# Kernel optimization log

Hardware: AMD Instinct MI355X
Metric: run time of the kernel (lower is better)

The kernel has to match this reference:

```python
import jax, jax.numpy as jnp
import numpy as np


def _sobel(img):
    # replicate-pad then Sobel cross-correlation (matches torch conv2d with wx, wy)
    p = jnp.pad(img, ((0, 0), (0, 0), (1, 1), (1, 1)), mode='edge')
    dx = ((p[:, :, 0:-2, 2:] - p[:, :, 0:-2, 0:-2])
          + 2.0 * (p[:, :, 1:-1, 2:] - p[:, :, 1:-1, 0:-2])
          + (p[:, :, 2:, 2:] - p[:, :, 2:, 0:-2]))
    dy = ((p[:, :, 2:, 0:-2] - p[:, :, 0:-2, 0:-2])
          + 2.0 * (p[:, :, 2:, 1:-1] - p[:, :, 0:-2, 1:-1])
          + (p[:, :, 2:, 2:] - p[:, :, 0:-2, 2:]))
    return dx, dy


def _compute_normal(vertex):
    # normal = normalize(dV/dx x dV/dy); zero out pixels at global min/max depth
    dx, dy = _sobel(vertex)
    n = jnp.cross(dx, dy, axis=1)                      # [B,3,H,W]
    mag = jnp.sqrt(jnp.sum(n * n, axis=1, keepdims=True) + 1e-16)
    n = n / (mag + 1e-8)
    depth = vertex[:, 2:3]
    invalid = (depth == depth.min()) | (depth == depth.max())
    return jnp.where(invalid, 0.0, n)


def _warp(feat, u, v):
    # bilinear sampling of feat [B,C,H,W] at (u,v) [B,N] -> [B,C,N]
    B, C, H, W = feat.shape
    u = jnp.clip(u, 0.0, W - 1.0)
    v = jnp.clip(v, 0.0, H - 1.0)
    u0 = jnp.floor(u); v0 = jnp.floor(v)
    wu = u - u0; wv = v - v0
    u0i = u0.astype(jnp.int32); v0i = v0.astype(jnp.int32)
    u1i = jnp.minimum(u0i + 1, W - 1); v1i = jnp.minimum(v0i + 1, H - 1)
    flat = feat.reshape(B, C, H * W)
    N = u.shape[-1]
    def g(ui, vi):
        idx = (vi * W + ui)[:, None, :]
        return jnp.take_along_axis(flat, jnp.broadcast_to(idx, (B, C, N)), axis=2)
    return (g(u0i, v0i) * ((1 - wu) * (1 - wv))[:, None]
            + g(u1i, v0i) * (wu * (1 - wv))[:, None]
            + g(u0i, v1i) * ((1 - wu) * wv)[:, None]
            + g(u1i, v1i) * (wu * wv)[:, None])


def _skew(v):  # [B,3] -> [B,3,3]
    x, y, z = v[..., 0], v[..., 1], v[..., 2]
    O = jnp.zeros_like(x)
    return jnp.stack([jnp.stack([O, -z, y], -1),
                      jnp.stack([z, O, -x], -1),
                      jnp.stack([-y, x, O], -1)], -2)


def _twist2mat(w):  # Rodrigues: so(3) [B,3] -> SO(3) [B,3,3]
    th = jnp.sqrt(jnp.sum(w * w, -1, keepdims=True) + 1e-24)
    Kv = _skew(w / th)
    th = th[..., None]
    I = jnp.eye(3, dtype=w.dtype)
    return I + jnp.sin(th) * Kv + (1.0 - jnp.cos(th)) * (Kv @ Kv)


def _icp_forward(depth0, depth1, K, R, t, max_iter=3):
    B, _, H, W = depth0.shape
    fx, fy, cx, cy = [K[:, i:i + 1] for i in range(4)]  # each [B,1]
    uu = jnp.arange(W, dtype=depth0.dtype)
    vv = jnp.arange(H, dtype=depth0.dtype)
    px = (uu[None, None, None, :] - cx[:, :, None, None]) / fx[:, :, None, None]
    py = (vv[None, None, :, None] - cy[:, :, None, None]) / fy[:, :, None, None]
    px = jnp.broadcast_to(px, (B, 1, H, W))
    py = jnp.broadcast_to(py, (B, 1, H, W))
    vertex0 = jnp.concatenate([px * depth0, py * depth0, depth0], 1)  # [B,3,H,W]
    vertex1 = jnp.concatenate([px * depth1, py * depth1, depth1], 1)
    normal0 = _compute_normal(vertex0)
    normal1 = _compute_normal(vertex1)
    N = H * W
    V0 = vertex0.reshape(B, 3, N)
    N0 = normal0.reshape(B, 3, N)
    P0 = V0.transpose(0, 2, 1)                          # [B,N,3]
    dpt0 = vertex0[:, 2].reshape(B, N)
    sigma_z = 0.0012 + 0.0019 * (dpt0 - 0.4) ** 2       # depth noise model
    eye6 = jnp.eye(6, dtype=depth0.dtype)
    for _ in range(max_iter):
        v0to1 = R @ V0 + t                               # [B,3,N]
        x_, y_, s_ = v0to1[:, 0], v0to1[:, 1], v0to1[:, 2]
        u_ = x_ / s_ * fx + cx
        v_ = y_ / s_ * fy + cy
        inviews = (u_ > 0) & (u_ < W - 1) & (v_ > 0) & (v_ < H - 1)
        rV1 = _warp(vertex1, u_, v_)                     # [B,3,N]
        rN1 = _warp(normal1, u_, v_)
        diff = v0to1 - rV1
        dnorm = jnp.sqrt(jnp.sum(diff * diff, axis=1) + 1e-16)
        occ = (~inviews) | (dnorm > 0.1)                 # [B,N]
        res = jnp.sum(rN1 * diff, axis=1)                # point-to-plane residual [B,N]
        NtC = jnp.einsum('bcn,bck->bnk', rN1, R)         # n_r^T R, [B,N,3]
        # n^T [p]_x == cross(n^T R, p)
        J = jnp.concatenate([jnp.cross(NtC, P0), -NtC], -1)  # [B,N,6]
        # sigma ~ |n_r . (R e_z)| * sigma_z (depth noise projected on normal)
        ndot = jnp.abs(jnp.sum(rN1 * R[:, :, 2][:, :, None], axis=1))
        sigma = ndot * sigma_z + 1e-3
        w_res = res / (sigma + 1e-8)
        J = -J / (sigma + 1e-8)[..., None]
        w_res = jnp.where(occ, 0.0, w_res)
        J = jnp.where(occ[..., None], 0.0, J)
        JtWJ = jnp.einsum('bnk,bnl->bkl', J, J)          # [B,6,6]
        JtR = jnp.einsum('bnk,bn->bk', J, w_res)[..., None]  # [B,6,1]
        tr = jnp.trace(JtWJ, axis1=1, axis2=2)
        Hlm = JtWJ + (tr * 1e-6)[:, None, None] * eye6   # LM damping
        xi = jnp.linalg.inv(Hlm) @ JtR                   # [B,6,1]
        dR = _twist2mat(-xi[:, :3, 0])
        dt = -(dR @ xi[:, 3:])
        R, t = R @ dR, R @ dt + t                        # inverse-compositional update
    weights = jnp.ones((B, 1, H, W), dtype=depth0.dtype)
    return R, t, weights


def setup_inputs() -> dict:
    key = jax.random.key(0)
    B, H, W = 16, 480, 640
    k1, k2, k3, k4 = jax.random.split(key, 4)
    TWO_PI = 6.2831853
    xs = jnp.linspace(0.0, 1.0, W, dtype=jnp.float32)
    ys = jnp.linspace(0.0, 1.0, H, dtype=jnp.float32)
    phase = jax.random.uniform(k1, (B, 1, 1, 1), minval=0.0, maxval=TWO_PI)
    # smooth positive depth surface so ICP inlier test keeps valid pixels
    depth0 = (2.0 + 0.5 * jnp.sin(TWO_PI * 3.0 * xs[None, None, None, :] + phase)
              * jnp.cos(TWO_PI * 2.0 * ys[None, None, :, None])).astype(jnp.float32)
    depth1 = depth0 + 0.01 * jax.random.normal(k2, (B, 1, H, W), dtype=jnp.float32)
    K = jnp.tile(jnp.array([[525.0, 525.0, 319.5, 239.5]], dtype=jnp.float32), (B, 1))
    w = 0.005 * jax.random.normal(k3, (B, 3), dtype=jnp.float32)
    R = _twist2mat(w)                                    # near-identity initial rotation
    t = 0.005 * jax.random.normal(k4, (B, 3, 1), dtype=jnp.float32)
    return {"depth0": depth0, "depth1": depth1, "K": K, "R": R, "t": t}


def reference(depth0, depth1, K, R, t):
    return _icp_forward(depth0, depth1, K, R, t, max_iter=3)
```

## Files before the change

### kernel.cpp

```cpp
#include <hip/hip_runtime.h>
#include <hip/hip_fp16.h>

#define IMH 480
#define IMW 640
#define HW (IMH*IMW)
#define NB 16

#define BPB 100
#define TPX 4
#define GROUPS 3
#define THREADS_PB (BPB*256)
#define GSTRIDE (THREADS_PB*TPX)
#define GROWS (GSTRIDE/IMW)

__device__ inline unsigned fenc(float x){
    unsigned u = __float_as_uint(x);
    return (u & 0x80000000u) ? ~u : (u | 0x80000000u);
}
__device__ inline float fdec(unsigned e){
    unsigned u = (e & 0x80000000u) ? (e & 0x7FFFFFFFu) : ~e;
    return __uint_as_float(u);
}

__global__ void init_kernel(const float* __restrict__ Rin, const float* __restrict__ tin,
                            float* __restrict__ stateR, float* __restrict__ statet,
                            unsigned* __restrict__ mm, float* __restrict__ acc){
    int i = threadIdx.x;
    if (i < NB*9) stateR[i] = Rin[i];
    if (i < NB*3) statet[i] = tin[i];
    if (i == 0){ mm[0] = 0xFFFFFFFFu; mm[1] = 0u; }
    for (int k = i; k < NB*27; k += 256) acc[k] = 0.f;
}

__global__ __launch_bounds__(256) void minmax_kernel(const float4* __restrict__ d, unsigned* __restrict__ mm){
    unsigned lmin = 0xFFFFFFFFu, lmax = 0u;
    const int total4 = NB*HW/4;
    for (int i = blockIdx.x*256 + threadIdx.x; i < total4; i += gridDim.x*256){
        float4 v = d[i];
        unsigned e0 = fenc(v.x), e1 = fenc(v.y), e2 = fenc(v.z), e3 = fenc(v.w);
        lmin = min(lmin, min(min(e0,e1), min(e2,e3)));
        lmax = max(lmax, max(max(e0,e1), max(e2,e3)));
    }
    #pragma unroll
    for (int off = 32; off; off >>= 1){
        lmin = min(lmin, (unsigned)__shfl_down((int)lmin, off));
        lmax = max(lmax, (unsigned)__shfl_down((int)lmax, off));
    }
    __shared__ unsigned smin[4], smax[4];
    int wave = threadIdx.x >> 6, lane = threadIdx.x & 63;
    if (lane == 0){ smin[wave] = lmin; smax[wave] = lmax; }
    __syncthreads();
    if (threadIdx.x == 0){
        unsigned bmin = min(min(smin[0],smin[1]), min(smin[2],smin[3]));
        unsigned bmax = max(max(smax[0],smax[1]), max(smax[2],smax[3]));
        atomicMin(&mm[0], bmin);
        atomicMax(&mm[1], bmax);
    }
}

__global__ __launch_bounds__(256) void normal_kernel(const float* __restrict__ depth1,
                                                     const float* __restrict__ Kp,
                                                     const unsigned* __restrict__ mm,
                                                     uint2* __restrict__ nrm,
                                                     float* __restrict__ weights){
    int b = blockIdx.y;
    int pix = blockIdx.x*256 + threadIdx.x;
    int r = pix / IMW, c = pix % IMW;
    const float fx = Kp[b*4+0], fy = Kp[b*4+1], cx = Kp[b*4+2], cy = Kp[b*4+3];
    const float inv_fx = 1.f/fx, inv_fy = 1.f/fy;
    const float* __restrict__ d = depth1 + (size_t)b*HW;
    int rm = max(r-1,0), rp = min(r+1,IMH-1), cm = max(c-1,0), cp = min(c+1,IMW-1);

    auto vert = [&](int rr, int cc, float v[3]){
        float dd = d[rr*IMW+cc];
        v[0] = ((float)cc - cx)*inv_fx*dd;
        v[1] = ((float)rr - cy)*inv_fy*dd;
        v[2] = dd;
    };
    float va[3],vb[3],vc2[3],vd[3],ve[3],vf[3],vg[3],vh[3];
    vert(rm,cm,va); vert(rm,c,vb);  vert(rm,cp,vc2);
    vert(r ,cm,vd);                 vert(r ,cp,ve);
    vert(rp,cm,vf); vert(rp,c,vg);  vert(rp,cp,vh);

    float dx[3], dy[3];
    #pragma unroll
    for (int k=0;k<3;k++){
        dx[k] = (vc2[k]-va[k]) + 2.f*(ve[k]-vd[k]) + (vh[k]-vf[k]);
        dy[k] = (vf[k]-va[k]) + 2.f*(vg[k]-vb[k]) + (vh[k]-vc2[k]);
    }
    float nx = dx[1]*dy[2] - dx[2]*dy[1];
    float ny = dx[2]*dy[0] - dx[0]*dy[2];
    float nz = dx[0]*dy[1] - dx[1]*dy[0];
    float mag = sqrtf(nx*nx + ny*ny + nz*nz + 1e-16f);
    float inv = __builtin_amdgcn_rcpf(mag + 1e-8f);
    nx *= inv; ny *= inv; nz *= inv;

    float dc = d[r*IMW+c];
    float dmin = fdec(mm[0]), dmax = fdec(mm[1]);
    if (dc == dmin || dc == dmax){ nx = 0.f; ny = 0.f; nz = 0.f; }

    __half2 hxy = __floats2half2_rn(nx, ny);
    __half2 hz0 = __floats2half2_rn(nz, 0.f);
    uint2 p;
    p.x = *reinterpret_cast<unsigned*>(&hxy);
    p.y = *reinterpret_cast<unsigned*>(&hz0);
    nrm[(size_t)b*HW + pix] = p;
    weights[(size_t)b*HW + pix] = 1.f;
}

__global__ __launch_bounds__(256) void iter_kernel(const float4* __restrict__ depth0_v4,
                                                   const float* __restrict__ depth1,
                                                   const uint2* __restrict__ nrm,
                                                   const float* __restrict__ Kp,
                                                   const float* __restrict__ stateR,
                                                   const float* __restrict__ statet,
                                                   float* __restrict__ acc){
    const int b = blockIdx.y;
    const float fx = Kp[b*4+0], fy = Kp[b*4+1], cx = Kp[b*4+2], cy = Kp[b*4+3];
    const float inv_fx = 1.f/fx, inv_fy = 1.f/fy;
    float Rm[9];
    #pragma unroll
    for (int i=0;i<9;i++) Rm[i] = stateR[b*9+i];
    float tv[3];
    #pragma unroll
    for (int i=0;i<3;i++) tv[i] = statet[b*3+i];

    const float4* __restrict__ d0v = depth0_v4 + (size_t)b*(HW/4);
    const float* __restrict__ d1   = depth1 + (size_t)b*HW;
    const uint2* __restrict__ nb_  = nrm + (size_t)b*HW;

    float accv[27];
    #pragma unroll
    for (int i=0;i<27;i++) accv[i] = 0.f;

    const int tid = blockIdx.x*256 + threadIdx.x;
    const int base0 = tid*TPX;
    const int c0 = base0 % IMW;
    const int r0 = base0 / IMW;
    const float px_base = ((float)c0 - cx)*inv_fx;
    float pyv = ((float)r0 - cy)*inv_fy;
    const float py_step = (float)GROWS*inv_fy;

    #pragma unroll 1
    for (int g = 0; g < GROUPS; g++){
        float4 d4 = d0v[tid + g*THREADS_PB];
        float dd[4] = {d4.x, d4.y, d4.z, d4.w};

        #pragma unroll
        for (int j = 0; j < TPX; j++){
            float d0 = dd[j];
            float V0x = (px_base + (float)j*inv_fx)*d0;
            float V0y = pyv*d0;
            float V0z = d0;

            float X = Rm[0]*V0x + Rm[1]*V0y + Rm[2]*V0z + tv[0];
            float Y = Rm[3]*V0x + Rm[4]*V0y + Rm[5]*V0z + tv[1];
            float Z = Rm[6]*V0x + Rm[7]*V0y + Rm[8]*V0z + tv[2];
            float invZ = __builtin_amdgcn_rcpf(Z);
            float uu = X*invZ*fx + cx;
            float vv = Y*invZ*fy + cy;

            bool inview = (uu > 0.f) && (uu < (float)(IMW-1)) && (vv > 0.f) && (vv < (float)(IMH-1));

            float J0=0.f,J1=0.f,J2=0.f,J3=0.f,J4=0.f,J5=0.f,wres=0.f;
            if (inview){
                float u0f = floorf(uu), v0f = floorf(vv);
                int u0 = (int)u0f, v0 = (int)v0f;
                float wu = uu - u0f, wv = vv - v0f;
                float w00 = (1.f-wu)*(1.f-wv), w10 = wu*(1.f-wv), w01 = (1.f-wu)*wv, w11 = wu*wv;
                int i00 = v0*IMW + u0;

                float d00 = d1[i00], d10 = d1[i00+1], d01 = d1[i00+IMW], d11 = d1[i00+IMW+1];
                uint2 h00 = nb_[i00], h10 = nb_[i00+1], h01 = nb_[i00+IMW], h11 = nb_[i00+IMW+1];

                float pxa = (u0f - cx)*inv_fx, pxb = pxa + inv_fx;
                float pya = (v0f - cy)*inv_fy, pyb = pya + inv_fy;
                float a = w00*d00, bb = w10*d10, cc = w01*d01, ee = w11*d11;
                float rVz = (a + bb) + (cc + ee);
                float rVx = (a + cc)*pxa + (bb + ee)*pxb;
                float rVy = (a + bb)*pya + (cc + ee)*pyb;

                float2 n00xy = __half22float2(*reinterpret_cast<__half2*>(&h00.x));
                float2 n00z_ = __half22float2(*reinterpret_cast<__half2*>(&h00.y));
                float2 n10xy = __half22float2(*reinterpret_cast<__half2*>(&h10.x));
                float2 n10z_ = __half22float2(*reinterpret_cast<__half2*>(&h10.y));
                float2 n01xy = __half22float2(*reinterpret_cast<__half2*>(&h01.x));
                float2 n01z_ = __half22float2(*reinterpret_cast<__half2*>(&h01.y));
                float2 n11xy = __half22float2(*reinterpret_cast<__half2*>(&h11.x));
                float2 n11z_ = __half22float2(*reinterpret_cast<__half2*>(&h11.y));

                float n0x = w00*n00xy.x + w10*n10xy.x + w01*n01xy.x + w11*n11xy.x;
                float n0y = w00*n00xy.y + w10*n10xy.y + w01*n01xy.y + w11*n11xy.y;
                float n0z = w00*n00z_.x + w10*n10z_.x + w01*n01z_.x + w11*n11z_.x;

                float dfx = X - rVx, dfy = Y - rVy, dfz = Z - rVz;
                float d2 = dfx*dfx + dfy*dfy + dfz*dfz + 1e-16f;
                if (d2 <= 0.01f){
                    float res = n0x*dfx + n0y*dfy + n0z*dfz;
                    float N0 = n0x*Rm[0] + n0y*Rm[3] + n0z*Rm[6];
                    float N1 = n0x*Rm[1] + n0y*Rm[4] + n0z*Rm[7];
                    float N2 = n0x*Rm[2] + n0y*Rm[5] + n0z*Rm[8];
                    float cr0 = N1*V0z - N2*V0y;
                    float cr1 = N2*V0x - N0*V0z;
                    float cr2 = N0*V0y - N1*V0x;
                    float ndot = fabsf(N2);
                    float dsh = d0 - 0.4f;
                    float sigz = 0.0012f + 0.0019f*dsh*dsh;
                    float sigma = ndot*sigz + 0.001f;
                    float invs = __builtin_amdgcn_rcpf(sigma + 1e-8f);
                    wres = res*invs;
                    J0 = -cr0*invs; J1 = -cr1*invs; J2 = -cr2*invs;
                    J3 =  N0*invs;  J4 =  N1*invs;  J5 =  N2*invs;
                }
            }

            float Jv[6] = {J0,J1,J2,J3,J4,J5};
            int idx = 0;
            #pragma unroll
            for (int k=0;k<6;k++)
                #pragma unroll
                for (int l=k;l<6;l++){ accv[idx] += Jv[k]*Jv[l]; idx++; }
            #pragma unroll
            for (int k=0;k<6;k++){ accv[idx] += Jv[k]*wres; idx++; }
        }

        pyv += py_step;
    }

    #pragma unroll
    for (int i=0;i<27;i++){
        float v = accv[i];
        #pragma unroll
        for (int off=32; off; off >>= 1) v += __shfl_down(v, off);
        accv[i] = v;
    }

    __shared__ float sacc[4][27];
    int wave = threadIdx.x >> 6, lane = threadIdx.x & 63;
    if (lane == 0){
        #pragma unroll
        for (int i=0;i<27;i++) sacc[wave][i] = accv[i];
    }
    __syncthreads();
    if (threadIdx.x < 27){
        float s = sacc[0][threadIdx.x] + sacc[1][threadIdx.x]
                + sacc[2][threadIdx.x] + sacc[3][threadIdx.x];
        atomicAdd(&acc[b*27 + threadIdx.x], s);
    }
}

__global__ void solve_kernel(float* __restrict__ acc,
                             float* __restrict__ stateR, float* __restrict__ statet,
                             float* __restrict__ outR, float* __restrict__ outt){
    int b = threadIdx.x;
    if (b >= NB) return;

    float a27[27];
    for (int i=0;i<27;i++) a27[i] = acc[b*27+i];
    for (int i=0;i<27;i++) acc[b*27+i] = 0.f;

    double A[6][6], rhs[6];
    int idx = 0;
    for (int k=0;k<6;k++)
        for (int l=k;l<6;l++){ A[k][l] = a27[idx]; A[l][k] = a27[idx]; idx++; }
    for (int k=0;k<6;k++) rhs[k] = a27[21+k];

    double tr = 0.0;
    for (int k=0;k<6;k++) tr += A[k][k];
    double lm = tr*1e-6;
    for (int k=0;k<6;k++) A[k][k] += lm;

    double M[6][7];
    for (int i=0;i<6;i++){ for (int j=0;j<6;j++) M[i][j]=A[i][j]; M[i][6]=rhs[i]; }
    for (int col=0; col<6; col++){
        int piv = col; double best = fabs(M[col][col]);
        for (int r2=col+1; r2<6; r2++){
            double v = fabs(M[r2][col]);
            if (v > best){ best = v; piv = r2; }
        }
        if (piv != col)
            for (int j=0;j<7;j++){ double tmp = M[col][j]; M[col][j] = M[piv][j]; M[piv][j] = tmp; }
        double p = M[col][col];
        for (int j=col;j<7;j++) M[col][j] /= p;
        for (int r2=0;r2<6;r2++){
            if (r2 == col) continue;
            double f = M[r2][col];
            for (int j=col;j<7;j++) M[r2][j] -= f*M[col][j];
        }
    }
    double xi[6];
    for (int k=0;k<6;k++) xi[k] = M[k][6];

    double w0 = -xi[0], w1 = -xi[1], w2 = -xi[2];
    double th = sqrt(w0*w0 + w1*w1 + w2*w2 + 1e-24);
    double kx = w0/th, ky = w1/th, kz = w2/th;
    double s = sin(th), cm1 = 1.0 - cos(th);
    double Kv[3][3] = {{0,-kz,ky},{kz,0,-kx},{-ky,kx,0}};
    double K2[3][3];
    for (int i=0;i<3;i++)
        for (int j=0;j<3;j++){
            double acc2 = 0.0;
            for (int k=0;k<3;k++) acc2 += Kv[i][k]*Kv[k][j];
            K2[i][j] = acc2;
        }
    double dR[3][3];
    for (int i=0;i<3;i++)
        for (int j=0;j<3;j++)
            dR[i][j] = (i==j ? 1.0 : 0.0) + s*Kv[i][j] + cm1*K2[i][j];
    double dt[3];
    for (int i=0;i<3;i++)
        dt[i] = -(dR[i][0]*xi[3] + dR[i][1]*xi[4] + dR[i][2]*xi[5]);

    double Ro[3][3];
    for (int i=0;i<3;i++) for (int j=0;j<3;j++) Ro[i][j] = (double)stateR[b*9 + i*3 + j];
    double to[3];
    for (int i=0;i<3;i++) to[i] = (double)statet[b*3+i];

    double Rn[3][3], tn[3];
    for (int i=0;i<3;i++)
        for (int j=0;j<3;j++){
            double acc2 = 0.0;
            for (int k=0;k<3;k++) acc2 += Ro[i][k]*dR[k][j];
            Rn[i][j] = acc2;
        }
    for (int i=0;i<3;i++)
        tn[i] = Ro[i][0]*dt[0] + Ro[i][1]*dt[1] + Ro[i][2]*dt[2] + to[i];

    for (int i=0;i<3;i++)
        for (int j=0;j<3;j++){
            float v = (float)Rn[i][j];
            stateR[b*9 + i*3 + j] = v;
            outR[b*9 + i*3 + j] = v;
        }
    for (int i=0;i<3;i++){
        float v = (float)tn[i];
        statet[b*3+i] = v;
        outt[b*3+i] = v;
    }
}

extern "C" void kernel_launch(void* const* d_in, const int* in_sizes, int n_in,
                              void* d_out, int out_size, void* d_ws, size_t ws_size,
                              hipStream_t stream){
    const float* depth0 = (const float*)d_in[0];
    const float* depth1 = (const float*)d_in[1];
    const float* Kp     = (const float*)d_in[2];
    const float* Rin    = (const float*)d_in[3];
    const float* tin    = (const float*)d_in[4];

    float* out     = (float*)d_out;
    float* outR    = out;
    float* outt    = out + NB*9;
    float* weights = out + NB*12;

    uint2* nrm     = (uint2*)d_ws;
    float* stateR  = (float*)(nrm + (size_t)NB*HW);
    float* statet  = stateR + NB*9;
    unsigned* mm   = (unsigned*)(statet + NB*3);
    float* acc     = (float*)(mm + 2);

    init_kernel<<<1, 256, 0, stream>>>(Rin, tin, stateR, statet, mm, acc);
    minmax_kernel<<<dim3(256), 256, 0, stream>>>((const float4*)depth1, mm);
    normal_kernel<<<dim3(HW/256, NB), 256, 0, stream>>>(depth1, Kp, mm, nrm, weights);
    for (int it = 0; it < 3; it++){
        iter_kernel<<<dim3(BPB, NB), 256, 0, stream>>>((const float4*)depth0, depth1, nrm, Kp, stateR, statet, acc);
        solve_kernel<<<1, 64, 0, stream>>>(acc, stateR, statet, outR, outt);
    }
}
```

Baseline: 251.9 us.

## Fuse 6x6 solve into iter kernel via last-block-done counter

```diff
diff --git a/kernel.cpp b/kernel.cpp
--- a/kernel.cpp
+++ b/kernel.cpp
@@ -24,11 +24,13 @@
 
 __global__ void init_kernel(const float* __restrict__ Rin, const float* __restrict__ tin,
                             float* __restrict__ stateR, float* __restrict__ statet,
-                            unsigned* __restrict__ mm, float* __restrict__ acc){
+                            unsigned* __restrict__ mm, float* __restrict__ acc,
+                            unsigned* __restrict__ cnt){
     int i = threadIdx.x;
     if (i < NB*9) stateR[i] = Rin[i];
     if (i < NB*3) statet[i] = tin[i];
     if (i == 0){ mm[0] = 0xFFFFFFFFu; mm[1] = 0u; }
+    if (i < NB) cnt[i] = 0u;
     for (int k = i; k < NB*27; k += 256) acc[k] = 0.f;
 }
 
@@ -112,9 +114,12 @@
                                                    const float* __restrict__ depth1,
                                                    const uint2* __restrict__ nrm,
                                                    const float* __restrict__ Kp,
-                                                   const float* __restrict__ stateR,
-                                                   const float* __restrict__ statet,
-                                                   float* __restrict__ acc){
+                                                   float* __restrict__ stateR,
+                                                   float* __restrict__ statet,
+                                                   float* __restrict__ acc,
+                                                   unsigned* __restrict__ cnt,
+                                                   float* __restrict__ outR,
+                                                   float* __restrict__ outt){
     const int b = blockIdx.y;
     const float fx = Kp[b*4+0], fy = Kp[b*4+1], cx = Kp[b*4+2], cy = Kp[b*4+3];
     const float inv_fx = 1.f/fx, inv_fy = 1.f/fy;
@@ -242,100 +247,86 @@
         for (int i=0;i<27;i++) sacc[wave][i] = accv[i];
     }
     __syncthreads();
+    float* __restrict__ accp = acc + b*27;
     if (threadIdx.x < 27){
         float s = sacc[0][threadIdx.x] + sacc[1][threadIdx.x]
                 + sacc[2][threadIdx.x] + sacc[3][threadIdx.x];
-        atomicAdd(&acc[b*27 + threadIdx.x], s);
-    }
-}
-
-__global__ void solve_kernel(float* __restrict__ acc,
-                             float* __restrict__ stateR, float* __restrict__ statet,
-                             float* __restrict__ outR, float* __restrict__ outt){
-    int b = threadIdx.x;
-    if (b >= NB) return;
-
-    float a27[27];
-    for (int i=0;i<27;i++) a27[i] = acc[b*27+i];
-    for (int i=0;i<27;i++) acc[b*27+i] = 0.f;
-
-    double A[6][6], rhs[6];
-    int idx = 0;
-    for (int k=0;k<6;k++)
-        for (int l=k;l<6;l++){ A[k][l] = a27[idx]; A[l][k] = a27[idx]; idx++; }
-    for (int k=0;k<6;k++) rhs[k] = a27[21+k];
-
-    double tr = 0.0;
-    for (int k=0;k<6;k++) tr += A[k][k];
-    double lm = tr*1e-6;
-    for (int k=0;k<6;k++) A[k][k] += lm;
-
-    double M[6][7];
-    for (int i=0;i<6;i++){ for (int j=0;j<6;j++) M[i][j]=A[i][j]; M[i][6]=rhs[i]; }
-    for (int col=0; col<6; col++){
-        int piv = col; double best = fabs(M[col][col]);
-        for (int r2=col+1; r2<6; r2++){
-            double v = fabs(M[r2][col]);
-            if (v > best){ best = v; piv = r2; }
+        atomicAdd(&accp[threadIdx.x], s);
+    }
+    __syncthreads();
+
+    __shared__ float Ms[6][7];
+    if (threadIdx.x == 0){
+        __threadfence();
+        unsigned old = atomicAdd(&cnt[b], 1u);
+        if (old == BPB - 1u){
+            float a27[27];
+            #pragma unroll
+            for (int i=0;i<27;i++) a27[i] = atomicAdd(&accp[i], 0.f);
+            #pragma unroll
+            for (int i=0;i<27;i++) accp[i] = 0.f;
+            cnt[b] = 0u;
+
+            int idx = 0;
+            for (int k=0;k<6;k++)
+                for (int l=k;l<6;l++){ Ms[k][l] = a27[idx]; Ms[l][k] = a27[idx]; idx++; }
+            float tr = 0.f;
+            for (int k=0;k<6;k++) tr += Ms[k][k];
+            float lm = tr*1e-6f;
+            for (int k=0;k<6;k++){ Ms[k][k] += lm; Ms[k][6] = a27[21+k]; }
+
+            for (int col=0; col<6; col++){
+                int piv = col; float best = fabsf(Ms[col][col]);
+                for (int r2=col+1; r2<6; r2++){
+                    float v = fabsf(Ms[r2][col]);
+                    if (v > best){ best = v; piv = r2; }
+                }
+                if (piv != col)
+                    for (int j=0;j<7;j++){ float tmp = Ms[col][j]; Ms[col][j] = Ms[piv][j]; Ms[piv][j] = tmp; }
+                float p = 1.f/Ms[col][col];
+                for (int j=col;j<7;j++) Ms[col][j] *= p;
+                for (int r2=0;r2<6;r2++){
+                    if (r2 == col) continue;
+                    float f = Ms[r2][col];
+                    for (int j=col;j<7;j++) Ms[r2][j] -= f*Ms[col][j];
+                }
+            }
+            float xi[6];
+            for (int k=0;k<6;k++) xi[k] = Ms[k][6];
+
+            float w0 = -xi[0], w1 = -xi[1], w2 = -xi[2];
+            float th = sqrtf(w0*w0 + w1*w1 + w2*w2 + 1e-24f);
+            float ith = 1.f/th;
+            float kx = w0*ith, ky = w1*ith, kz = w2*ith;
+            float s = sinf(th), cm1 = 1.f - cosf(th);
+            float dRm[9];
+            dRm[0] = 1.f + cm1*(-ky*ky - kz*kz);
+            dRm[1] = -s*kz + cm1*(kx*ky);
+            dRm[2] =  s*ky + cm1*(kx*kz);
+            dRm[3] =  s*kz + cm1*(kx*ky);
+            dRm[4] = 1.f + cm1*(-kx*kx - kz*kz);
+            dRm[5] = -s*kx + cm1*(ky*kz);
+            dRm[6] = -s*ky + cm1*(kx*kz);
+            dRm[7] =  s*kx + cm1*(ky*kz);
+            dRm[8] = 1.f + cm1*(-kx*kx - ky*ky);
+
+            float dt0 = -(dRm[0]*xi[3] + dRm[1]*xi[4] + dRm[2]*xi[5]);
+            float dt1 = -(dRm[3]*xi[3] + dRm[4]*xi[4] + dRm[5]*xi[5]);
+            float dt2 = -(dRm[6]*xi[3] + dRm[7]*xi[4] + dRm[8]*xi[5]);
+
+            float Rn[9];
+            for (int i=0;i<3;i++)
+                for (int j=0;j<3;j++)
+                    Rn[i*3+j] = Rm[i*3+0]*dRm[0*3+j] + Rm[i*3+1]*dRm[1*3+j] + Rm[i*3+2]*dRm[2*3+j];
+            float tn0 = Rm[0]*dt0 + Rm[1]*dt1 + Rm[2]*dt2 + tv[0];
+            float tn1 = Rm[3]*dt0 + Rm[4]*dt1 + Rm[5]*dt2 + tv[1];
+            float tn2 = Rm[6]*dt0 + Rm[7]*dt1 + Rm[8]*dt2 + tv[2];
+
+            for (int i=0;i<9;i++){ stateR[b*9+i] = Rn[i]; outR[b*9+i] = Rn[i]; }
+            statet[b*3+0] = tn0; outt[b*3+0] = tn0;
+            statet[b*3+1] = tn1; outt[b*3+1] = tn1;
+            statet[b*3+2] = tn2; outt[b*3+2] = tn2;
         }
-        if (piv != col)
-            for (int j=0;j<7;j++){ double tmp = M[col][j]; M[col][j] = M[piv][j]; M[piv][j] = tmp; }
-        double p = M[col][col];
-        for (int j=col;j<7;j++) M[col][j] /= p;
-        for (int r2=0;r2<6;r2++){
-            if (r2 == col) continue;
-            double f = M[r2][col];
-            for (int j=col;j<7;j++) M[r2][j] -= f*M[col][j];
-        }
-    }
-    double xi[6];
-    for (int k=0;k<6;k++) xi[k] = M[k][6];
-
-    double w0 = -xi[0], w1 = -xi[1], w2 = -xi[2];
-    double th = sqrt(w0*w0 + w1*w1 + w2*w2 + 1e-24);
-    double kx = w0/th, ky = w1/th, kz = w2/th;
-    double s = sin(th), cm1 = 1.0 - cos(th);
-    double Kv[3][3] = {{0,-kz,ky},{kz,0,-kx},{-ky,kx,0}};
-    double K2[3][3];
-    for (int i=0;i<3;i++)
-        for (int j=0;j<3;j++){
-            double acc2 = 0.0;
-            for (int k=0;k<3;k++) acc2 += Kv[i][k]*Kv[k][j];
-            K2[i][j] = acc2;
-        }
-    double dR[3][3];
-    for (int i=0;i<3;i++)
-        for (int j=0;j<3;j++)
-            dR[i][j] = (i==j ? 1.0 : 0.0) + s*Kv[i][j] + cm1*K2[i][j];
-    double dt[3];
-    for (int i=0;i<3;i++)
-        dt[i] = -(dR[i][0]*xi[3] + dR[i][1]*xi[4] + dR[i][2]*xi[5]);
-
-    double Ro[3][3];
-    for (int i=0;i<3;i++) for (int j=0;j<3;j++) Ro[i][j] = (double)stateR[b*9 + i*3 + j];
-    double to[3];
-    for (int i=0;i<3;i++) to[i] = (double)statet[b*3+i];
-
-    double Rn[3][3], tn[3];
-    for (int i=0;i<3;i++)
-        for (int j=0;j<3;j++){
-            double acc2 = 0.0;
-            for (int k=0;k<3;k++) acc2 += Ro[i][k]*dR[k][j];
-            Rn[i][j] = acc2;
-        }
-    for (int i=0;i<3;i++)
-        tn[i] = Ro[i][0]*dt[0] + Ro[i][1]*dt[1] + Ro[i][2]*dt[2] + to[i];
-
-    for (int i=0;i<3;i++)
-        for (int j=0;j<3;j++){
-            float v = (float)Rn[i][j];
-            stateR[b*9 + i*3 + j] = v;
-            outR[b*9 + i*3 + j] = v;
-        }
-    for (int i=0;i<3;i++){
-        float v = (float)tn[i];
-        statet[b*3+i] = v;
-        outt[b*3+i] = v;
     }
 }
 
@@ -358,12 +349,13 @@
     float* statet  = stateR + NB*9;
     unsigned* mm   = (unsigned*)(statet + NB*3);
     float* acc     = (float*)(mm + 2);
-
-    init_kernel<<<1, 256, 0, stream>>>(Rin, tin, stateR, statet, mm, acc);
-    minmax_kernel<<<dim3(256), 256, 0, stream>>>((const float4*)depth1, mm);
+    unsigned* cnt  = (unsigned*)(acc + NB*27);
+
+    init_kernel<<<1, 256, 0, stream>>>(Rin, tin, stateR, statet, mm, acc, cnt);
+    minmax_kernel<<<dim3(512), 256, 0, stream>>>((const float4*)depth1, mm);
     normal_kernel<<<dim3(HW/256, NB), 256, 0, stream>>>(depth1, Kp, mm, nrm, weights);
     for (int it = 0; it < 3; it++){
-        iter_kernel<<<dim3(BPB, NB), 256, 0, stream>>>((const float4*)depth0, depth1, nrm, Kp, stateR, statet, acc);
-        solve_kernel<<<1, 64, 0, stream>>>(acc, stateR, statet, outR, outt);
-    }
-}
+        iter_kernel<<<dim3(BPB, NB), 256, 0, stream>>>((const float4*)depth0, depth1, nrm, Kp,
+                                                       stateR, statet, acc, cnt, outR, outt);
+    }
+}
```

After: 367.3 us. 45.8% more time.
